# Optimization experiments

Hardware: AMD Instinct MI355X
Metric: run time of the kernel (lower is better)

The kernel has to match this reference:

```python
import jax, jax.numpy as jnp
import numpy as np


def _affine_grid(params, B, H, W):
    # torch F.affine_grid semantics, align_corners=False
    tx = params[:, 0] / W
    ty = params[:, 1] / H
    theta = params[:, 2]
    c = jnp.cos(theta)[:, None, None]   # (B,1,1)
    s = jnp.sin(theta)[:, None, None]
    # base normalized coords (pixel-center convention for align_corners=False)
    xs = (2.0 * jnp.arange(W, dtype=params.dtype) + 1.0) / W - 1.0  # (W,)
    ys = (2.0 * jnp.arange(H, dtype=params.dtype) + 1.0) / H - 1.0  # (H,)
    xs = xs[None, None, :]   # (1,1,W)
    ys = ys[None, :, None]   # (1,H,1)
    gx = c * xs - s * ys + tx[:, None, None]  # (B,H,W)
    gy = s * xs + c * ys + ty[:, None, None]  # (B,H,W)
    return gx, gy


def _bilinear_sample_one(im, gx, gy):
    # im: (C,H,W); gx,gy: (H,W) normalized coords in [-1,1]
    # grid_sample align_corners=False, padding_mode='zeros'
    C, H, W = im.shape
    ix = ((gx + 1.0) * W - 1.0) * 0.5
    iy = ((gy + 1.0) * H - 1.0) * 0.5
    x0f = jnp.floor(ix)
    y0f = jnp.floor(iy)
    x0 = x0f.astype(jnp.int32)
    y0 = y0f.astype(jnp.int32)
    x1 = x0 + 1
    y1 = y0 + 1
    wx1 = ix - x0f
    wx0 = 1.0 - wx1
    wy1 = iy - y0f
    wy0 = 1.0 - wy1

    def gather(yc, xc):
        valid = ((xc >= 0) & (xc < W) & (yc >= 0) & (yc < H)).astype(im.dtype)
        xcc = jnp.clip(xc, 0, W - 1)
        ycc = jnp.clip(yc, 0, H - 1)
        return im[:, ycc, xcc] * valid[None]  # (C,H,W)

    out = (gather(y0, x0) * (wy0 * wx0)[None]
           + gather(y0, x1) * (wy0 * wx1)[None]
           + gather(y1, x0) * (wy1 * wx0)[None]
           + gather(y1, x1) * (wy1 * wx1)[None])
    return out


def setup_inputs() -> dict:
    key = jax.random.key(0)
    k1, k2 = jax.random.split(key)
    img = jax.random.normal(k1, (16, 8, 512, 512), dtype=jnp.float32)
    params = jax.random.normal(k2, (16, 3), dtype=jnp.float32)
    return {"img": img, "params": params}


def reference(img, params):
    B, C, H, W = img.shape
    gx, gy = _affine_grid(params, B, H, W)  # (B,H,W) each
    return jax.vmap(_bilinear_sample_one)(img, gx, gy)  # (B,C,H,W)
```

## Files before the change

### kernel.cpp

```cpp
#include <hip/hip_runtime.h>
#include <math.h>

constexpr int B = 16, C = 8, H = 512, W = 512;
constexpr int HW = H * W;
constexpr int TILE = 32;
constexpr int ROWS = 48;
constexpr int LSTR = 79;
constexpr int BUFSZ = ROWS * LSTR;

__device__ __forceinline__ void dma4(const float* g, float* l) {
    __builtin_amdgcn_global_load_lds(
        (const __attribute__((address_space(1))) unsigned int*)g,
        (__attribute__((address_space(3))) unsigned int*)l,
        4, 0, 0);
}

__global__ __launch_bounds__(256, 8) void grid_sampler_kernel(
    const float* __restrict__ img,
    const float* __restrict__ params,
    float* __restrict__ out) {
    __shared__ float lds[BUFSZ];
    const int tid = threadIdx.x;

    const int blk = (int)blockIdx.x;
    const int l   = (blk & 7) * 4096 + (blk >> 3);
    const int b   = l >> 11;
    const int ch  = (l >> 8) & 7;
    const int tt  = l & 255;
    const int ty0 = (tt >> 4) * TILE;
    const int tx0 = (tt & 15) * TILE;

    if (tid < ROWS) lds[tid * LSTR + 64] = 0.0f;

    const float tpx = params[b * 3 + 0] * (1.0f / W);
    const float tpy = params[b * 3 + 1] * (1.0f / H);
    const float th  = params[b * 3 + 2];
    const float c = cosf(th), s = sinf(th);

    auto srcxy = [&](float x, float y, float& ix, float& iy) {
        float xs = (2.0f * x + 1.0f) * (1.0f / W) - 1.0f;
        float ys = (2.0f * y + 1.0f) * (1.0f / H) - 1.0f;
        float gx = c * xs - s * ys + tpx;
        float gy = s * xs + c * ys + tpy;
        ix = ((gx + 1.0f) * (float)W - 1.0f) * 0.5f;
        iy = ((gy + 1.0f) * (float)H - 1.0f) * 0.5f;
    };

    float ixa, iya, ixb, iyb, ixc, iyc, ixd, iyd;
    srcxy((float)tx0,             (float)ty0,             ixa, iya);
    srcxy((float)(tx0 + TILE-1),  (float)ty0,             ixb, iyb);
    srcxy((float)tx0,             (float)(ty0 + TILE-1),  ixc, iyc);
    srcxy((float)(tx0 + TILE-1),  (float)(ty0 + TILE-1),  ixd, iyd);
    const float ixmin = fminf(fminf(ixa, ixb), fminf(ixc, ixd));
    const float iymin = fminf(fminf(iya, iyb), fminf(iyc, iyd));
    const int xlo = min(max((int)floorf(ixmin), 0), W - 1);
    const int ylo = min(max((int)floorf(iymin), 0), H - 1);
    const int xls = xlo - 1;
    const int yls = min(ylo, H - ROWS);

    const size_t plane = (size_t)(b * C + ch) * HW;
    const int wv = tid >> 6, ln = tid & 63;
    const int scol = min(max(xls + ln, 0), W - 1);
    const float* sbase = img + plane + (size_t)yls * W + scol;
#pragma unroll
    for (int j2 = 0; j2 < 12; ++j2) {
        const int r = 12 * wv + j2;
        dma4(sbase + (size_t)r * W, &lds[r * LSTR]);
    }

    const int oy  = ty0 + (tid >> 3);
    const int oxb = tx0 + (tid & 7) * 4;

    asm volatile("s_waitcnt vmcnt(0) lgkmcnt(0)\n\ts_barrier" ::: "memory");

    float4 v;
#pragma unroll
    for (int j = 0; j < 4; ++j) {
        float ix, iy;
        srcxy((float)(oxb + j), (float)oy, ix, iy);
        const float x0f = floorf(ix), y0f = floorf(iy);
        const int x0 = (int)x0f, y0 = (int)y0f;
        const int x1 = x0 + 1,  y1 = y0 + 1;
        const float wx1 = ix - x0f, wx0 = 1.0f - wx1;
        const float wy1 = iy - y0f, wy0 = 1.0f - wy1;
        const float vx0 = (x0 >= 0 && x0 < W) ? 1.0f : 0.0f;
        const float vx1 = (x1 >= 0 && x1 < W) ? 1.0f : 0.0f;
        const float vy0 = (y0 >= 0 && y0 < H) ? 1.0f : 0.0f;
        const float vy1 = (y1 >= 0 && y1 < H) ? 1.0f : 0.0f;
        const float w00 = wy0 * wx0 * vy0 * vx0;
        const float w01 = wy0 * wx1 * vy0 * vx1;
        const float w10 = wy1 * wx0 * vy1 * vx0;
        const float w11 = wy1 * wx1 * vy1 * vx1;
        const int xi  = min(max(x0 - xls, 0), 63);
        const int yi0 = min(max(y0 - yls, 0), ROWS - 1);
        const int yi1 = min(max(y1 - yls, 0), ROWS - 1);
        const int a0 = yi0 * LSTR + xi;
        const int a1 = yi1 * LSTR + xi;
        const float t00 = lds[a0], t01 = lds[a0 + 1];
        const float t10 = lds[a1], t11 = lds[a1 + 1];
        ((float*)&v)[j] = t00 * w00 + t01 * w01 + t10 * w10 + t11 * w11;
    }
    *(float4*)(out + plane + oy * W + oxb) = v;
}

extern "C" void kernel_launch(void* const* d_in, const int* in_sizes, int n_in,
                              void* d_out, int out_size, void* d_ws, size_t ws_size,
                              hipStream_t stream) {
    const float* img    = (const float*)d_in[0];
    const float* params = (const float*)d_in[1];
    float*       out    = (float*)d_out;

    constexpr int grid = B * C * (H / TILE) * (W / TILE);
    grid_sampler_kernel<<<grid, 256, 0, stream>>>(img, params, out);
}
```

Before: 249.1 us.

## Replace LDS tile staging with direct gathers reusing weights across channels

Drops the per-channel LDS staging of a 48x64 source window through global_load_lds. Each block now computes the bilinear offsets and weights once per output pixel and loops over all 8 channels, gathering the four neighbours straight from global memory. The grid shrinks by a factor of C and the occupancy hint drops from 8 to 6. This removes redundant coordinate math and the LDS barrier. In exchange the gathers are uncoalesced, relying on L1/L2 for reuse, and there is less parallelism per launch.

```diff
diff --git a/kernel.cpp b/kernel.cpp
--- a/kernel.cpp
+++ b/kernel.cpp
@@ -4,33 +4,19 @@
 constexpr int B = 16, C = 8, H = 512, W = 512;
 constexpr int HW = H * W;
 constexpr int TILE = 32;
-constexpr int ROWS = 48;
-constexpr int LSTR = 79;
-constexpr int BUFSZ = ROWS * LSTR;
 
-__device__ __forceinline__ void dma4(const float* g, float* l) {
-    __builtin_amdgcn_global_load_lds(
-        (const __attribute__((address_space(1))) unsigned int*)g,
-        (__attribute__((address_space(3))) unsigned int*)l,
-        4, 0, 0);
-}
-
-__global__ __launch_bounds__(256, 8) void grid_sampler_kernel(
+__global__ __launch_bounds__(256, 6) void grid_sampler_kernel(
     const float* __restrict__ img,
     const float* __restrict__ params,
     float* __restrict__ out) {
-    __shared__ float lds[BUFSZ];
     const int tid = threadIdx.x;
 
     const int blk = (int)blockIdx.x;
-    const int l   = (blk & 7) * 4096 + (blk >> 3);
-    const int b   = l >> 11;
-    const int ch  = (l >> 8) & 7;
+    const int l   = (blk & 7) * 512 + (blk >> 3);
+    const int b   = l >> 8;
     const int tt  = l & 255;
     const int ty0 = (tt >> 4) * TILE;
     const int tx0 = (tt & 15) * TILE;
-
-    if (tid < ROWS) lds[tid * LSTR + 64] = 0.0f;
 
     const float tpx = params[b * 3 + 0] * (1.0f / W);
     const float tpy = params[b * 3 + 1] * (1.0f / H);
@@ -46,34 +32,11 @@
         iy = ((gy + 1.0f) * (float)H - 1.0f) * 0.5f;
     };
 
-    float ixa, iya, ixb, iyb, ixc, iyc, ixd, iyd;
-    srcxy((float)tx0,             (float)ty0,             ixa, iya);
-    srcxy((float)(tx0 + TILE-1),  (float)ty0,             ixb, iyb);
-    srcxy((float)tx0,             (float)(ty0 + TILE-1),  ixc, iyc);
-    srcxy((float)(tx0 + TILE-1),  (float)(ty0 + TILE-1),  ixd, iyd);
-    const float ixmin = fminf(fminf(ixa, ixb), fminf(ixc, ixd));
-    const float iymin = fminf(fminf(iya, iyb), fminf(iyc, iyd));
-    const int xlo = min(max((int)floorf(ixmin), 0), W - 1);
-    const int ylo = min(max((int)floorf(iymin), 0), H - 1);
-    const int xls = xlo - 1;
-    const int yls = min(ylo, H - ROWS);
-
-    const size_t plane = (size_t)(b * C + ch) * HW;
-    const int wv = tid >> 6, ln = tid & 63;
-    const int scol = min(max(xls + ln, 0), W - 1);
-    const float* sbase = img + plane + (size_t)yls * W + scol;
-#pragma unroll
-    for (int j2 = 0; j2 < 12; ++j2) {
-        const int r = 12 * wv + j2;
-        dma4(sbase + (size_t)r * W, &lds[r * LSTR]);
-    }
-
     const int oy  = ty0 + (tid >> 3);
     const int oxb = tx0 + (tid & 7) * 4;
 
-    asm volatile("s_waitcnt vmcnt(0) lgkmcnt(0)\n\ts_barrier" ::: "memory");
-
-    float4 v;
+    int   o00[4], o01[4], o10[4], o11[4];
+    float w00[4], w01[4], w10[4], w11[4];
 #pragma unroll
     for (int j = 0; j < 4; ++j) {
         float ix, iy;
@@ -87,20 +50,34 @@
         const float vx1 = (x1 >= 0 && x1 < W) ? 1.0f : 0.0f;
         const float vy0 = (y0 >= 0 && y0 < H) ? 1.0f : 0.0f;
         const float vy1 = (y1 >= 0 && y1 < H) ? 1.0f : 0.0f;
-        const float w00 = wy0 * wx0 * vy0 * vx0;
-        const float w01 = wy0 * wx1 * vy0 * vx1;
-        const float w10 = wy1 * wx0 * vy1 * vx0;
-        const float w11 = wy1 * wx1 * vy1 * vx1;
-        const int xi  = min(max(x0 - xls, 0), 63);
-        const int yi0 = min(max(y0 - yls, 0), ROWS - 1);
-        const int yi1 = min(max(y1 - yls, 0), ROWS - 1);
-        const int a0 = yi0 * LSTR + xi;
-        const int a1 = yi1 * LSTR + xi;
-        const float t00 = lds[a0], t01 = lds[a0 + 1];
-        const float t10 = lds[a1], t11 = lds[a1 + 1];
-        ((float*)&v)[j] = t00 * w00 + t01 * w01 + t10 * w10 + t11 * w11;
+        w00[j] = wy0 * wx0 * vy0 * vx0;
+        w01[j] = wy0 * wx1 * vy0 * vx1;
+        w10[j] = wy1 * wx0 * vy1 * vx0;
+        w11[j] = wy1 * wx1 * vy1 * vx1;
+        const int x0c = min(max(x0, 0), W - 1);
+        const int x1c = min(max(x1, 0), W - 1);
+        const int y0c = min(max(y0, 0), H - 1);
+        const int y1c = min(max(y1, 0), H - 1);
+        const int r0 = y0c * W, r1 = y1c * W;
+        o00[j] = r0 + x0c;  o01[j] = r0 + x1c;
+        o10[j] = r1 + x0c;  o11[j] = r1 + x1c;
     }
-    *(float4*)(out + plane + oy * W + oxb) = v;
+
+    const float* ip = img + (size_t)b * C * HW;
+    float*       op = out + (size_t)b * C * HW;
+    const int ooff = oy * W + oxb;
+    for (int k = 0; k < C; ++k) {
+        float4 v;
+#pragma unroll
+        for (int j = 0; j < 4; ++j) {
+            const float t00 = ip[o00[j]], t01 = ip[o01[j]];
+            const float t10 = ip[o10[j]], t11 = ip[o11[j]];
+            ((float*)&v)[j] = t00 * w00[j] + t01 * w01[j]
+                            + t10 * w10[j] + t11 * w11[j];
+        }
+        *(float4*)(op + ooff) = v;
+        ip += HW; op += HW;
+    }
 }
 
 extern "C" void kernel_launch(void* const* d_in, const int* in_sizes, int n_in,
@@ -110,6 +87,6 @@
     const float* params = (const float*)d_in[1];
     float*       out    = (float*)d_out;
 
-    constexpr int grid = B * C * (H / TILE) * (W / TILE);
+    constexpr int grid = B * (H / TILE) * (W / TILE);
     grid_sampler_kernel<<<grid, 256, 0, stream>>>(img, params, out);
 }
```

Result: slower. 358.4 us (+43.9%).
